# Optimization experiments

Measured on AMD Instinct MI355X. Metric: run time of the kernel, lower is better.

## Reference

```python
import jax, jax.numpy as jnp
import numpy as np

D_MODEL, N_LEVELS, N_HEADS, N_POINTS = 256, 4, 8, 4
HEAD_DIM = D_MODEL // N_HEADS
SPATIAL = [(100, 100), (50, 50), (25, 25), (13, 13)]  # (H, W) per level
BATCH = 2


def setup_inputs() -> dict:
    key = jax.random.key(0)
    ks = jax.random.split(key, 10)
    len_in = sum(h * w for h, w in SPATIAL)
    n, lq = BATCH, len_in
    s = 0.02
    mlp = N_HEADS * N_LEVELS * N_POINTS
    starts = np.cumsum([0] + [h * w for h, w in SPATIAL])[:-1]
    return {
        "query": jax.random.normal(ks[0], (n, lq, D_MODEL), jnp.float32),
        "reference_points": jax.random.uniform(ks[1], (n, lq, N_LEVELS, 2), jnp.float32),
        "input_flatten": jax.random.normal(ks[2], (n, len_in, D_MODEL), jnp.float32),
        "input_spatial_shapes": jnp.array(SPATIAL, dtype=jnp.int32),
        "input_level_start_index": jnp.array(starts, dtype=jnp.int32),
        "Wv": jax.random.normal(ks[3], (D_MODEL, D_MODEL), jnp.float32) * s,
        "bv": jnp.zeros((D_MODEL,), jnp.float32),
        "Woff": jax.random.normal(ks[4], (D_MODEL, mlp * 2), jnp.float32) * s,
        "boff": jax.random.normal(ks[5], (mlp * 2,), jnp.float32) * s,
        "Wattn": jax.random.normal(ks[6], (D_MODEL, mlp), jnp.float32) * s,
        "battn": jnp.zeros((mlp,), jnp.float32),
        "Wout": jax.random.normal(ks[7], (D_MODEL, D_MODEL), jnp.float32) * s,
        "bout": jnp.zeros((D_MODEL,), jnp.float32),
    }


def _ms_deform_attn_core(value, spatial_shapes, loc, aw):
    """value [N,S,M,D]; loc [N,Lq,M,L,P,2] in [0,1]; aw [N,Lq,M,L,P] -> [N,Lq,M*D].
    Faithful to F.grid_sample(mode='bilinear', padding_mode='zeros', align_corners=False)."""
    n, lq, m, L, p, _ = loc.shape
    d = value.shape[-1]
    out = jnp.zeros((n, m, lq, d), value.dtype)
    gather = jax.vmap(jax.vmap(lambda v, i: v[i]))  # vmap over N and M
    start = 0
    for lvl, (H, W) in enumerate(spatial_shapes):
        v = value[:, start:start + H * W].transpose(0, 2, 1, 3)  # [N,M,HW,D]
        start += H * W
        # align_corners=False: grid g=2*loc-1 -> pixel = ((g+1)*size-1)/2 = loc*size-0.5
        x = loc[:, :, :, lvl, :, 0] * W - 0.5  # [N,Lq,M,P]
        y = loc[:, :, :, lvl, :, 1] * H - 0.5
        x0 = jnp.floor(x)
        y0 = jnp.floor(y)
        wx = x - x0
        wy = y - y0
        x0i = x0.astype(jnp.int32)
        y0i = y0.astype(jnp.int32)
        samp = jnp.zeros((n, m, lq * p, d), value.dtype)
        for dy, wyc in ((0, 1.0 - wy), (1, wy)):
            for dx, wxc in ((0, 1.0 - wx), (1, wx)):
                xi = x0i + dx
                yi = y0i + dy
                valid = (xi >= 0) & (xi < W) & (yi >= 0) & (yi < H)  # zeros padding
                idx = jnp.clip(yi, 0, H - 1) * W + jnp.clip(xi, 0, W - 1)
                idx = idx.transpose(0, 2, 1, 3).reshape(n, m, lq * p)
                w = (wxc * wyc * valid).transpose(0, 2, 1, 3).reshape(n, m, lq * p)
                samp = samp + gather(v, idx) * w[..., None]
        samp = samp.reshape(n, m, lq, p, d)
        aw_l = aw[:, :, :, lvl, :].transpose(0, 2, 1, 3)  # [N,M,Lq,P]
        out = out + (samp * aw_l[..., None]).sum(3)
    return out.transpose(0, 2, 1, 3).reshape(n, lq, m * d)


def reference(query, reference_points, input_flatten, input_spatial_shapes,
              input_level_start_index, Wv, bv, Woff, boff, Wattn, battn, Wout, bout):
    n, lq, _ = query.shape
    m, L, p = N_HEADS, N_LEVELS, N_POINTS
    shapes = np.asarray(input_spatial_shapes)  # concrete/static [L,2] = (H,W)
    value = (input_flatten @ Wv + bv).reshape(n, -1, m, HEAD_DIM)
    off = (query @ Woff + boff).reshape(n, lq, m, L, p, 2)
    aw = jax.nn.softmax((query @ Wattn + battn).reshape(n, lq, m, L * p), axis=-1)
    aw = aw.reshape(n, lq, m, L, p)
    norm = jnp.asarray(shapes[:, ::-1].astype(np.float32))  # [L,2] = (W,H)
    loc = reference_points[:, :, None, :, None, :] + off / norm[None, None, None, :, None, :]
    out = _ms_deform_attn_core(value, [tuple(s) for s in shapes.tolist()], loc, aw)
    return out @ Wout + bout
```

## Files before the change

### kernel.cpp

```cpp
#include <hip/hip_runtime.h>
#include <hip/hip_bf16.h>

#define NB    2
#define LQ    13294
#define DM    256
#define NH    8
#define HD    32
#define NL    4
#define NP    4
#define ROWS  (NB*LQ)

#define OFF_VALUE 0u
#define OFF_TMP   13613056u
#define OFF_OFFS  27226112u
#define OFF_AWL   54452224u
#define OFF_WT    61258752u
#define OFF_FLAG  61717504u

#define WT_WV    0
#define WT_WOFF  65536
#define WT_WATTN 131072
#define WT_WOUT  163840

#define BSTR 264

typedef __attribute__((ext_vector_type(8))) short short8;
typedef __attribute__((ext_vector_type(4))) float floatx4;

static __device__ __forceinline__ float blo(int u)  { return __uint_as_float(((unsigned)u) << 16); }
static __device__ __forceinline__ float bhif(int u) { return __uint_as_float(((unsigned)u) & 0xffff0000u); }

static __device__ __forceinline__ int pack_bf2(float a, float b) {
    __hip_bfloat162 h(__float2bfloat16(a), __float2bfloat16(b));
    int u; __builtin_memcpy(&u, &h, 4); return u;
}

static __device__ __forceinline__ float load_bias(const void* b, int i, int flag) {
    return flag ? __bfloat162float(((const __hip_bfloat16*)b)[i]) : ((const float*)b)[i];
}

static __device__ __forceinline__ short8 load_afrag(const void* A, int row, int k, bool a_bf) {
    if (a_bf) {
        return *(const short8*)((const short*)A + row * 256 + k);
    } else {
        const float* p = (const float*)A + row * 256 + k;
        float4 f0 = *(const float4*)p, f1 = *(const float4*)(p + 4);
        int4 pk; pk.x = pack_bf2(f0.x, f0.y); pk.y = pack_bf2(f0.z, f0.w);
                 pk.z = pack_bf2(f1.x, f1.y); pk.w = pack_bf2(f1.z, f1.w);
        short8 r; __builtin_memcpy(&r, &pk, 16); return r;
    }
}

__global__ void sniff_k(const unsigned int* __restrict__ q, int* __restrict__ flag) {
    const int t = threadIdx.x;
    int hits = 0;
#pragma unroll
    for (int i = 0; i < 4; ++i) {
        unsigned lo = q[t * 4 + i] & 0xffffu;
        unsigned e  = (lo >> 7) & 0xffu;
        if ((e >= 110u && e <= 132u) || lo == 0u) ++hits;
    }
#pragma unroll
    for (int s = 1; s < 64; s <<= 1) hits += __shfl_xor(hits, s);
    if (t == 0) *flag = (hits > 160) ? 1 : 0;
}

__global__ __launch_bounds__(256) void trans_k(
    const void* __restrict__ s0, const void* __restrict__ s1,
    const void* __restrict__ s2, const void* __restrict__ s3,
    short* __restrict__ wt, const int* __restrict__ flagp)
{
    const int flag = *flagp;
    const int z = blockIdx.z;
    const void* src = (z == 0) ? s0 : (z == 1) ? s1 : (z == 2) ? s2 : s3;
    short* dst = wt + ((z == 0) ? WT_WV : (z == 1) ? WT_WOFF : (z == 2) ? WT_WATTN : WT_WOUT);
    const int N = (z == 2) ? 128 : 256;
    const int n0 = blockIdx.x * 32, k0 = blockIdx.y * 32;
    if (n0 >= N) return;

    __shared__ short tile[32 * 36];
    const int t = threadIdx.x;
    const int r = t >> 3, c4 = (t & 7) * 4;
    if (flag) {
        const short* sp = (const short*)src + (k0 + r) * N + n0 + c4;
        *(short4*)&tile[r * 36 + c4] = *(const short4*)sp;
    } else {
        const float* sp = (const float*)src + (k0 + r) * N + n0 + c4;
        float4 v = *(const float4*)sp;
        short4 o;
        o.x = (short)(pack_bf2(v.x, v.x) & 0xffff);
        o.y = (short)(pack_bf2(v.y, v.y) & 0xffff);
        o.z = (short)(pack_bf2(v.z, v.z) & 0xffff);
        o.w = (short)(pack_bf2(v.w, v.w) & 0xffff);
        *(short4*)&tile[r * 36 + c4] = o;
    }
    __syncthreads();
    const int nn = t >> 3, r4 = (t & 7) * 4;
    short4 o;
    o.x = tile[(r4 + 0) * 36 + nn];
    o.y = tile[(r4 + 1) * 36 + nn];
    o.z = tile[(r4 + 2) * 36 + nn];
    o.w = tile[(r4 + 3) * 36 + nn];
    *(short4*)&dst[(n0 + nn) * 256 + k0 + r4] = o;
}

__global__ __launch_bounds__(256) void gemm_front_k(
    const void* __restrict__ flat, const void* __restrict__ query,
    const short* __restrict__ wt,
    const void* __restrict__ bv, const void* __restrict__ boff, const void* __restrict__ battn,
    short* __restrict__ value, float* __restrict__ offsb, short* __restrict__ awl,
    const int* __restrict__ flagp)
{
    const int  flag = *flagp;
    const bool a_bf = (flag != 0);

    __shared__ __align__(16) short Bs[128 * BSTR];

    const int tid = threadIdx.x;
    const int bx = blockIdx.x;
    const bool isv = (bx < 2);
    const void*  A   = isv ? flat : query;
    const short* Wtb = isv ? (wt + WT_WV) : (wt + WT_WOFF);
    const int colbase = (isv ? bx : bx - 2) * 128;
    const int bm = blockIdx.y * 128;

#pragma unroll
    for (int i = 0; i < 16; ++i) {
        const int ch = i * 256 + tid;
        const int c = ch >> 5, ks = (ch & 31) * 8;
        *(int4*)&Bs[c * BSTR + ks] = *(const int4*)(Wtb + (colbase + c) * 256 + ks);
    }
    __syncthreads();

    const int w = tid >> 6, lane = tid & 63;
    const int qd = lane >> 4, ln = lane & 15;
    const int m0 = bm + w * 32;
    const int r0 = min(m0 + ln, ROWS - 1);
    const int r1 = min(m0 + 16 + ln, ROWS - 1);

    floatx4 acc[2][8];
#pragma unroll
    for (int i = 0; i < 2; ++i)
#pragma unroll
        for (int j = 0; j < 8; ++j) acc[i][j] = floatx4{0.f, 0.f, 0.f, 0.f};

#pragma unroll
    for (int k0 = 0; k0 < 256; k0 += 32) {
        const int kk = k0 + qd * 8;
        const short8 af0 = load_afrag(A, r0, kk, a_bf);
        const short8 af1 = load_afrag(A, r1, kk, a_bf);
#pragma unroll
        for (int j = 0; j < 8; ++j) {
            const short8 bf = *(const short8*)&Bs[(j * 16 + ln) * BSTR + kk];
            acc[0][j] = __builtin_amdgcn_mfma_f32_16x16x32_bf16(af0, bf, acc[0][j], 0, 0, 0);
            acc[1][j] = __builtin_amdgcn_mfma_f32_16x16x32_bf16(af1, bf, acc[1][j], 0, 0, 0);
        }
    }

#pragma unroll
    for (int j = 0; j < 8; ++j) {
        const int col = colbase + j * 16 + ln;
        float bj;
        if (isv)            bj = load_bias(bv, col, flag);
        else if (col < 256) bj = load_bias(boff, col, flag);
        else                bj = load_bias(battn, col - 256, flag);
#pragma unroll
        for (int i = 0; i < 2; ++i) {
#pragma unroll
            for (int r = 0; r < 4; ++r) {
                const int row = m0 + i * 16 + qd * 4 + r;
                if (row >= ROWS) continue;
                const float v = acc[i][j][r] + bj;
                if (isv)            value[row * 256 + col] = (short)(pack_bf2(v, v) & 0xffff);
                else if (col < 256) offsb[row * 256 + col] = v;
                else                awl[row * 128 + col - 256] = (short)(pack_bf2(v, v) & 0xffff);
            }
        }
    }
}

__global__ __launch_bounds__(256) void gemm_out_k(
    const short* __restrict__ tmp, const short* __restrict__ wtout,
    const void* __restrict__ bout, void* __restrict__ C,
    const int* __restrict__ flagp)
{
    const int flag = *flagp;

    __shared__ __align__(16) short Bs[64 * BSTR];

    const int tid = threadIdx.x;
    const int colbase = blockIdx.x * 64;
    const int bm = blockIdx.y * 128;

#pragma unroll
    for (int i = 0; i < 8; ++i) {
        const int ch = i * 256 + tid;
        const int c = ch >> 5, ks = (ch & 31) * 8;
        *(int4*)&Bs[c * BSTR + ks] = *(const int4*)(wtout + (colbase + c) * 256 + ks);
    }
    __syncthreads();

    const int w = tid >> 6, lane = tid & 63;
    const int qd = lane >> 4, ln = lane & 15;
    const int m0 = bm + w * 32;
    const int r0 = min(m0 + ln, ROWS - 1);
    const int r1 = min(m0 + 16 + ln, ROWS - 1);

    floatx4 acc[2][4];
#pragma unroll
    for (int i = 0; i < 2; ++i)
#pragma unroll
        for (int j = 0; j < 4; ++j) acc[i][j] = floatx4{0.f, 0.f, 0.f, 0.f};

#pragma unroll
    for (int k0 = 0; k0 < 256; k0 += 32) {
        const int kk = k0 + qd * 8;
        const short8 af0 = *(const short8*)(tmp + r0 * 256 + kk);
        const short8 af1 = *(const short8*)(tmp + r1 * 256 + kk);
#pragma unroll
        for (int j = 0; j < 4; ++j) {
            const short8 bf = *(const short8*)&Bs[(j * 16 + ln) * BSTR + kk];
            acc[0][j] = __builtin_amdgcn_mfma_f32_16x16x32_bf16(af0, bf, acc[0][j], 0, 0, 0);
            acc[1][j] = __builtin_amdgcn_mfma_f32_16x16x32_bf16(af1, bf, acc[1][j], 0, 0, 0);
        }
    }

#pragma unroll
    for (int j = 0; j < 4; ++j) {
        const int col = colbase + j * 16 + ln;
        const float bj = load_bias(bout, col, flag);
#pragma unroll
        for (int i = 0; i < 2; ++i) {
#pragma unroll
            for (int r = 0; r < 4; ++r) {
                const int row = m0 + i * 16 + qd * 4 + r;
                if (row >= ROWS) continue;
                const float v = acc[i][j][r] + bj;
                if (flag) ((__hip_bfloat16*)C)[row * 256 + col] = __float2bfloat16(v);
                else      ((float*)C)[row * 256 + col] = v;
            }
        }
    }
}

__global__ __launch_bounds__(256) void sampler_k(
    const void* __restrict__ refp, const short* __restrict__ value,
    const float* __restrict__ offs, const short* __restrict__ awl,
    short* __restrict__ tmp, const int* __restrict__ flagp)
{
    const int flag = *flagp;
    const int nq = blockIdx.x * 4 + (threadIdx.x >> 6);
    const int lane = threadIdx.x & 63;
    const int h = lane >> 3, u = lane & 7;
    const int n = (nq >= LQ) ? 1 : 0;

    const int lg = *(const int*)(awl + nq * 128 + h * 16 + u * 2);
    float l0 = blo(lg), l1 = bhif(lg);
    float m = fmaxf(l0, l1);
    m = fmaxf(m, __shfl_xor(m, 1));
    m = fmaxf(m, __shfl_xor(m, 2));
    m = fmaxf(m, __shfl_xor(m, 4));
    float e0 = __expf(l0 - m), e1 = __expf(l1 - m);
    float s = e0 + e1;
    s += __shfl_xor(s, 1);
    s += __shfl_xor(s, 2);
    s += __shfl_xor(s, 4);
    const float inv = 1.f / s;
    const float w0 = e0 * inv, w1 = e1 * inv;

    const float4 of = *(const float4*)(offs + nq * 256 + h * 32 + u * 4);

    float rxl, ryl;
    if (flag) {
        const int rr = *(const int*)((const short*)refp + nq * 8 + (u & 3) * 2);
        rxl = blo(rr); ryl = bhif(rr);
    } else {
        const float* rp = (const float*)refp + nq * 8 + (u & 3) * 2;
        rxl = rp[0]; ryl = rp[1];
    }

    const short* vb = value + (n ? LQ * 256 : 0) + h * 32 + u * 4;

    float a0 = 0.f, a1 = 0.f, a2 = 0.f, a3 = 0.f;

    const int WlA[NL] = {100, 50, 25, 13};
    const int StA[NL] = {0, 10000, 12500, 13125};

#pragma unroll
    for (int idx = 0; idx < 16; ++idx) {
        const int l = idx >> 2;
        const int Wl = WlA[l];
        const float Wf = (float)Wl;
        const int owner = h * 8 + (idx >> 1);
        const float ox = __shfl((idx & 1) ? of.z : of.x, owner);
        const float oy = __shfl((idx & 1) ? of.w : of.y, owner);
        const float wa = __shfl((idx & 1) ? w1 : w0, owner);
        const float rx = __shfl(rxl, h * 8 + l);
        const float ry = __shfl(ryl, h * 8 + l);

        const float px = fmaf(rx, Wf, ox) - 0.5f;
        const float py = fmaf(ry, Wf, oy) - 0.5f;
        const float x0f = floorf(px), y0f = floorf(py);
        const float wx = px - x0f, wy = py - y0f;
        const int x0 = (int)x0f, y0 = (int)y0f;
        const short* vl = vb + StA[l] * 256;

#pragma unroll
        for (int dy = 0; dy < 2; ++dy) {
#pragma unroll
            for (int dx = 0; dx < 2; ++dx) {
                const int xi = x0 + dx, yi = y0 + dy;
                const bool vld = (xi >= 0) & (xi < Wl) & (yi >= 0) & (yi < Wl);
                const float wgt = (dx ? wx : 1.f - wx) * (dy ? wy : 1.f - wy);
                const float ww = vld ? wa * wgt : 0.f;
                const int xc = min(max(xi, 0), Wl - 1);
                const int yc = min(max(yi, 0), Wl - 1);
                const int2 raw = *(const int2*)(vl + (yc * Wl + xc) * 256);
                a0 = fmaf(ww, blo(raw.x),  a0);
                a1 = fmaf(ww, bhif(raw.x), a1);
                a2 = fmaf(ww, blo(raw.y),  a2);
                a3 = fmaf(ww, bhif(raw.y), a3);
            }
        }
    }

    int2 o;
    o.x = pack_bf2(a0, a1);
    o.y = pack_bf2(a2, a3);
    *(int2*)(tmp + nq * 256 + h * 32 + u * 4) = o;
}

extern "C" void kernel_launch(void* const* d_in, const int* in_sizes, int n_in,
                              void* d_out, int out_size, void* d_ws, size_t ws_size,
                              hipStream_t stream)
{
    const void* query  = d_in[0];
    const void* refpts = d_in[1];
    const void* flat   = d_in[2];
    const void* Wv     = d_in[5];
    const void* bv     = d_in[6];
    const void* Woff   = d_in[7];
    const void* boff   = d_in[8];
    const void* Wattn  = d_in[9];
    const void* battn  = d_in[10];
    const void* Wout   = d_in[11];
    const void* bout   = d_in[12];

    char* ws = (char*)d_ws;
    short* value = (short*)(ws + OFF_VALUE);
    short* tmp   = (short*)(ws + OFF_TMP);
    float* offsb = (float*)(ws + OFF_OFFS);
    short* awl   = (short*)(ws + OFF_AWL);
    short* wt    = (short*)(ws + OFF_WT);
    int*   flagp = (int*)(ws + OFF_FLAG);

    const int gmy = (ROWS + 127) / 128;

    sniff_k<<<1, 64, 0, stream>>>((const unsigned int*)query, flagp);
    trans_k<<<dim3(8, 8, 4), 256, 0, stream>>>(Wv, Woff, Wattn, Wout, wt, flagp);
    gemm_front_k<<<dim3(5, gmy), 256, 0, stream>>>(flat, query, wt, bv, boff, battn,
                                                   value, offsb, awl, flagp);
    sampler_k<<<ROWS / 4, 256, 0, stream>>>(refpts, value, offsb, awl, tmp, flagp);
    gemm_out_k<<<dim3(4, gmy), 256, 0, stream>>>(tmp, wt + WT_WOUT, bout, d_out, flagp);
}
```

Baseline: 246.8 us.

## Stage GEMM A tiles through double-buffered swizzled LDS with direct global-to-LDS loads

Both GEMM kernels now stage A fragments into a double-buffered LDS tile and load B with direct global-to-LDS copies into an XOR-swizzled layout, replacing per-lane global A loads and padded B storage. Each wave now computes a 64x64 sub-tile instead of 32 rows by the full width, which raises register-level reuse. The output GEMM moves to 128-column tiles, halving its grid. The cost is more LDS per block, which may lower occupancy, plus a barrier per K step. When the input is fp32 the A path still converts in registers and writes LDS with ordinary stores.

New measurement: 252.4 us. 2.2% more time.

```diff
diff --git a/kernel.cpp b/kernel.cpp
--- a/kernel.cpp
+++ b/kernel.cpp
@@ -22,8 +22,6 @@
 #define WT_WATTN 131072
 #define WT_WOUT  163840
 
-#define BSTR 264
-
 typedef __attribute__((ext_vector_type(8))) short short8;
 typedef __attribute__((ext_vector_type(4))) float floatx4;
 
@@ -39,16 +37,10 @@
     return flag ? __bfloat162float(((const __hip_bfloat16*)b)[i]) : ((const float*)b)[i];
 }
 
-static __device__ __forceinline__ short8 load_afrag(const void* A, int row, int k, bool a_bf) {
-    if (a_bf) {
-        return *(const short8*)((const short*)A + row * 256 + k);
-    } else {
-        const float* p = (const float*)A + row * 256 + k;
-        float4 f0 = *(const float4*)p, f1 = *(const float4*)(p + 4);
-        int4 pk; pk.x = pack_bf2(f0.x, f0.y); pk.y = pack_bf2(f0.z, f0.w);
-                 pk.z = pack_bf2(f1.x, f1.y); pk.w = pack_bf2(f1.z, f1.w);
-        short8 r; __builtin_memcpy(&r, &pk, 16); return r;
-    }
+static __device__ __forceinline__ void gload_lds16(const void* g, void* l) {
+    __builtin_amdgcn_global_load_lds(
+        (const __attribute__((address_space(1))) unsigned*)g,
+        (__attribute__((address_space(3))) unsigned*)l, 16, 0, 0);
 }
 
 __global__ void sniff_k(const unsigned int* __restrict__ q, int* __restrict__ flag) {
@@ -114,9 +106,12 @@
     const int  flag = *flagp;
     const bool a_bf = (flag != 0);
 
-    __shared__ __align__(16) short Bs[128 * BSTR];
+    __shared__ __align__(16) short Bs[128 * 256];
+    __shared__ __align__(16) short As[2][128 * 32];
 
     const int tid = threadIdx.x;
+    const int w = tid >> 6, lane = tid & 63;
+    const int qd = lane >> 4, ln = lane & 15;
     const int bx = blockIdx.x;
     const bool isv = (bx < 2);
     const void*  A   = isv ? flat : query;
@@ -125,50 +120,77 @@
     const int bm = blockIdx.y * 128;
 
 #pragma unroll
-    for (int i = 0; i < 16; ++i) {
-        const int ch = i * 256 + tid;
-        const int c = ch >> 5, ks = (ch & 31) * 8;
-        *(int4*)&Bs[c * BSTR + ks] = *(const int4*)(Wtb + (colbase + c) * 256 + ks);
-    }
+    for (int r = 0; r < 16; ++r) {
+        const int c = r * 256 + tid;
+        const int col = c >> 5;
+        const int kc = (c & 31) ^ (col & 31);
+        gload_lds16(Wtb + (colbase + col) * 256 + kc * 8, &Bs[(r * 256 + w * 64) * 8]);
+    }
+
+    auto stage_a = [&](int buf, int k0) {
+#pragma unroll
+        for (int r = 0; r < 2; ++r) {
+            const int c = r * 256 + tid;
+            const int row = min(bm + (c >> 2), ROWS - 1);
+            const int kc = ((c & 3) ^ ((c >> 2) & 3)) * 8;
+            if (a_bf) {
+                gload_lds16((const short*)A + row * 256 + k0 + kc,
+                            &As[buf][(r * 256 + w * 64) * 8]);
+            } else {
+                const float* p = (const float*)A + row * 256 + k0 + kc;
+                float4 f0 = *(const float4*)p, f1 = *(const float4*)(p + 4);
+                int4 pk; pk.x = pack_bf2(f0.x, f0.y); pk.y = pack_bf2(f0.z, f0.w);
+                         pk.z = pack_bf2(f1.x, f1.y); pk.w = pack_bf2(f1.z, f1.w);
+                *(int4*)&As[buf][c * 8] = pk;
+            }
+        }
+    };
+    stage_a(0, 0);
     __syncthreads();
 
-    const int w = tid >> 6, lane = tid & 63;
-    const int qd = lane >> 4, ln = lane & 15;
-    const int m0 = bm + w * 32;
-    const int r0 = min(m0 + ln, ROWS - 1);
-    const int r1 = min(m0 + 16 + ln, ROWS - 1);
-
-    floatx4 acc[2][8];
-#pragma unroll
-    for (int i = 0; i < 2; ++i)
-#pragma unroll
-        for (int j = 0; j < 8; ++j) acc[i][j] = floatx4{0.f, 0.f, 0.f, 0.f};
-
-#pragma unroll
-    for (int k0 = 0; k0 < 256; k0 += 32) {
-        const int kk = k0 + qd * 8;
-        const short8 af0 = load_afrag(A, r0, kk, a_bf);
-        const short8 af1 = load_afrag(A, r1, kk, a_bf);
-#pragma unroll
-        for (int j = 0; j < 8; ++j) {
-            const short8 bf = *(const short8*)&Bs[(j * 16 + ln) * BSTR + kk];
-            acc[0][j] = __builtin_amdgcn_mfma_f32_16x16x32_bf16(af0, bf, acc[0][j], 0, 0, 0);
-            acc[1][j] = __builtin_amdgcn_mfma_f32_16x16x32_bf16(af1, bf, acc[1][j], 0, 0, 0);
-        }
-    }
-
-#pragma unroll
-    for (int j = 0; j < 8; ++j) {
-        const int col = colbase + j * 16 + ln;
+    const int wm = (w & 1) * 64, wn = (w >> 1) * 64;
+
+    floatx4 acc[4][4];
+#pragma unroll
+    for (int i = 0; i < 4; ++i)
+#pragma unroll
+        for (int j = 0; j < 4; ++j) acc[i][j] = floatx4{0.f, 0.f, 0.f, 0.f};
+
+#pragma unroll
+    for (int i0 = 0; i0 < 8; ++i0) {
+        if (i0 < 7) stage_a((i0 + 1) & 1, 32 * (i0 + 1));
+        const short* Ab = As[i0 & 1];
+        short8 af[4], bf[4];
+#pragma unroll
+        for (int i = 0; i < 4; ++i) {
+            const int row = wm + i * 16 + ln;
+            af[i] = *(const short8*)&Ab[(row * 4 + (qd ^ (row & 3))) * 8];
+        }
+#pragma unroll
+        for (int j = 0; j < 4; ++j) {
+            const int col = wn + j * 16 + ln;
+            bf[j] = *(const short8*)&Bs[(col * 32 + ((4 * i0 + qd) ^ (col & 31))) * 8];
+        }
+#pragma unroll
+        for (int i = 0; i < 4; ++i)
+#pragma unroll
+            for (int j = 0; j < 4; ++j)
+                acc[i][j] = __builtin_amdgcn_mfma_f32_16x16x32_bf16(af[i], bf[j], acc[i][j], 0, 0, 0);
+        if (i0 < 7) __syncthreads();
+    }
+
+#pragma unroll
+    for (int j = 0; j < 4; ++j) {
+        const int col = colbase + wn + j * 16 + ln;
         float bj;
         if (isv)            bj = load_bias(bv, col, flag);
         else if (col < 256) bj = load_bias(boff, col, flag);
         else                bj = load_bias(battn, col - 256, flag);
 #pragma unroll
-        for (int i = 0; i < 2; ++i) {
+        for (int i = 0; i < 4; ++i) {
 #pragma unroll
             for (int r = 0; r < 4; ++r) {
-                const int row = m0 + i * 16 + qd * 4 + r;
+                const int row = bm + wm + i * 16 + qd * 4 + r;
                 if (row >= ROWS) continue;
                 const float v = acc[i][j][r] + bj;
                 if (isv)            value[row * 256 + col] = (short)(pack_bf2(v, v) & 0xffff);
@@ -186,54 +208,75 @@
 {
     const int flag = *flagp;
 
-    __shared__ __align__(16) short Bs[64 * BSTR];
+    __shared__ __align__(16) short Bs[128 * 256];
+    __shared__ __align__(16) short As[2][128 * 32];
 
     const int tid = threadIdx.x;
-    const int colbase = blockIdx.x * 64;
-    const int bm = blockIdx.y * 128;
-
-#pragma unroll
-    for (int i = 0; i < 8; ++i) {
-        const int ch = i * 256 + tid;
-        const int c = ch >> 5, ks = (ch & 31) * 8;
-        *(int4*)&Bs[c * BSTR + ks] = *(const int4*)(wtout + (colbase + c) * 256 + ks);
-    }
-    __syncthreads();
-
     const int w = tid >> 6, lane = tid & 63;
     const int qd = lane >> 4, ln = lane & 15;
-    const int m0 = bm + w * 32;
-    const int r0 = min(m0 + ln, ROWS - 1);
-    const int r1 = min(m0 + 16 + ln, ROWS - 1);
-
-    floatx4 acc[2][4];
-#pragma unroll
-    for (int i = 0; i < 2; ++i)
+    const int colbase = blockIdx.x * 128;
+    const int bm = blockIdx.y * 128;
+
+#pragma unroll
+    for (int r = 0; r < 16; ++r) {
+        const int c = r * 256 + tid;
+        const int col = c >> 5;
+        const int kc = (c & 31) ^ (col & 31);
+        gload_lds16(wtout + (colbase + col) * 256 + kc * 8, &Bs[(r * 256 + w * 64) * 8]);
+    }
+
+    auto stage_a = [&](int buf, int k0) {
+#pragma unroll
+        for (int r = 0; r < 2; ++r) {
+            const int c = r * 256 + tid;
+            const int row = min(bm + (c >> 2), ROWS - 1);
+            const int kc = ((c & 3) ^ ((c >> 2) & 3)) * 8;
+            gload_lds16(tmp + row * 256 + k0 + kc, &As[buf][(r * 256 + w * 64) * 8]);
+        }
+    };
+    stage_a(0, 0);
+    __syncthreads();
+
+    const int wm = (w & 1) * 64, wn = (w >> 1) * 64;
+
+    floatx4 acc[4][4];
+#pragma unroll
+    for (int i = 0; i < 4; ++i)
 #pragma unroll
         for (int j = 0; j < 4; ++j) acc[i][j] = floatx4{0.f, 0.f, 0.f, 0.f};
 
 #pragma unroll
-    for (int k0 = 0; k0 < 256; k0 += 32) {
-        const int kk = k0 + qd * 8;
-        const short8 af0 = *(const short8*)(tmp + r0 * 256 + kk);
-        const short8 af1 = *(const short8*)(tmp + r1 * 256 + kk);
+    for (int i0 = 0; i0 < 8; ++i0) {
+        if (i0 < 7) stage_a((i0 + 1) & 1, 32 * (i0 + 1));
+        const short* Ab = As[i0 & 1];
+        short8 af[4], bf[4];
+#pragma unroll
+        for (int i = 0; i < 4; ++i) {
+            const int row = wm + i * 16 + ln;
+            af[i] = *(const short8*)&Ab[(row * 4 + (qd ^ (row & 3))) * 8];
+        }
 #pragma unroll
         for (int j = 0; j < 4; ++j) {
-            const short8 bf = *(const short8*)&Bs[(j * 16 + ln) * BSTR + kk];
-            acc[0][j] = __builtin_amdgcn_mfma_f32_16x16x32_bf16(af0, bf, acc[0][j], 0, 0, 0);
-            acc[1][j] = __builtin_amdgcn_mfma_f32_16x16x32_bf16(af1, bf, acc[1][j], 0, 0, 0);
-        }
+            const int col = wn + j * 16 + ln;
+            bf[j] = *(const short8*)&Bs[(col * 32 + ((4 * i0 + qd) ^ (col & 31))) * 8];
+        }
+#pragma unroll
+        for (int i = 0; i < 4; ++i)
+#pragma unroll
+            for (int j = 0; j < 4; ++j)
+                acc[i][j] = __builtin_amdgcn_mfma_f32_16x16x32_bf16(af[i], bf[j], acc[i][j], 0, 0, 0);
+        if (i0 < 7) __syncthreads();
     }
 
 #pragma unroll
     for (int j = 0; j < 4; ++j) {
-        const int col = colbase + j * 16 + ln;
+        const int col = colbase + wn + j * 16 + ln;
         const float bj = load_bias(bout, col, flag);
 #pragma unroll
-        for (int i = 0; i < 2; ++i) {
+        for (int i = 0; i < 4; ++i) {
 #pragma unroll
             for (int r = 0; r < 4; ++r) {
-                const int row = m0 + i * 16 + qd * 4 + r;
+                const int row = bm + wm + i * 16 + qd * 4 + r;
                 if (row >= ROWS) continue;
                 const float v = acc[i][j][r] + bj;
                 if (flag) ((__hip_bfloat16*)C)[row * 256 + col] = __float2bfloat16(v);
@@ -361,5 +404,5 @@
     gemm_front_k<<<dim3(5, gmy), 256, 0, stream>>>(flat, query, wt, bv, boff, battn,
                                                    value, offsb, awl, flagp);
     sampler_k<<<ROWS / 4, 256, 0, stream>>>(refpts, value, offsb, awl, tmp, flagp);
-    gemm_out_k<<<dim3(4, gmy), 256, 0, stream>>>(tmp, wt + WT_WOUT, bout, d_out, flagp);
-}
+    gemm_out_k<<<dim3(2, gmy), 256, 0, stream>>>(tmp, wt + WT_WOUT, bout, d_out, flagp);
+}
```
